# Performance work log

Measured on AMD Instinct MI355X. Metric: run time of the kernel, lower is better.

Reference implementation:

```python
import jax, jax.numpy as jnp
import numpy as np

N = 200000
B = 1024          # batch_size (number of graphs/segments)
D = 256           # in_channels
STEPS = 3         # processing_steps


def setup_inputs() -> dict:
    key = jax.random.key(0)
    ks = jax.random.split(key, 6)
    x = jax.random.normal(ks[0], (N, D), dtype=jnp.float32)
    bank_kg = jnp.zeros((1,), dtype=jnp.float32)  # unused by forward
    batch = jnp.sort(jax.random.randint(ks[1], (N,), 0, B, dtype=jnp.int32))
    q_star = jax.random.normal(ks[2], (B, 2 * D), dtype=jnp.float32)
    s = 1.0 / np.sqrt(D)  # PyTorch LSTM init scale
    W_ih = jax.random.uniform(ks[3], (4 * D, 2 * D), jnp.float32, -s, s)
    W_hh = jax.random.uniform(ks[4], (4 * D, D), jnp.float32, -s, s)
    b_ih = jnp.zeros((4 * D,), dtype=jnp.float32)
    b_hh = jnp.zeros((4 * D,), dtype=jnp.float32)
    return {"x": x, "bank_kg": bank_kg, "batch": batch, "q_star": q_star,
            "W_ih": W_ih, "W_hh": W_hh, "b_ih": b_ih, "b_hh": b_hh}


def _lstm_cell(inp, h, c, W_ih, W_hh, b_ih, b_hh):
    # PyTorch gate order: i, f, g, o
    gates = inp @ W_ih.T + b_ih + h @ W_hh.T + b_hh  # [B, 4D]
    i, f, g, o = jnp.split(gates, 4, axis=-1)
    i = jax.nn.sigmoid(i)
    f = jax.nn.sigmoid(f)
    g = jnp.tanh(g)
    o = jax.nn.sigmoid(o)
    c = f * c + i * g
    h = o * jnp.tanh(c)
    return h, c


def _segment_softmax(e, batch, num_segments):
    # numerically stable softmax over nodes grouped by segment id
    emax = jax.ops.segment_max(e, batch, num_segments=num_segments)
    emax = jnp.where(jnp.isfinite(emax), emax, 0.0)  # guard empty segments
    ee = jnp.exp(e - emax[batch])
    denom = jax.ops.segment_sum(ee, batch, num_segments=num_segments)
    return ee / (denom[batch] + 1e-16)


def reference(x, bank_kg, batch, q_star, W_ih, W_hh, b_ih, b_hh):
    del bank_kg  # unused in the original forward
    h = jnp.zeros((B, D), dtype=x.dtype)
    c = jnp.zeros((B, D), dtype=x.dtype)
    for _ in range(STEPS):
        h, c = _lstm_cell(q_star, h, c, W_ih, W_hh, b_ih, b_hh)
        q = h                                       # [B, D]
        e = jnp.sum(x * q[batch], axis=-1)          # [N] attention logits
        a = _segment_softmax(e, batch, B)           # [N]
        r = jax.ops.segment_sum(a[:, None] * x, batch, num_segments=B)  # [B, D]
        q_star = jnp.concatenate([q, r], axis=-1)   # [B, 2D]
    return q_star
```

## Files before the change

### kernel.cpp

```cpp
#include <hip/hip_runtime.h>
#include <hip/hip_bf16.h>
#include <cstdint>


#define NN     200000
#define BSEG   1024
#define DD     256
#define KA     768
#define FOURD  1024

using bf16x8 = __attribute__((ext_vector_type(8))) __bf16;
using f32x4  = __attribute__((ext_vector_type(4))) float;

__device__ __forceinline__ float bf2f(unsigned int u) {
  union { unsigned int i; float f; } v; v.i = (u & 0xffffu) << 16; return v.f;
}
__device__ __forceinline__ unsigned short f2bf(float f) {
  union { float f; unsigned int i; } v; v.f = f;
  unsigned int x = v.i;
  if ((x & 0x7fffffffu) > 0x7f800000u) return (unsigned short)((x >> 16) | 0x40);
  return (unsigned short)((x + 0x7fffu + ((x >> 16) & 1u)) >> 16);
}
__device__ __forceinline__ void split_bf(float f, unsigned short& hi, unsigned short& lo) {
  hi = f2bf(f);
  lo = f2bf(f - bf2f(hi));
}


__global__ void seg_bounds(const int* __restrict__ batch, int* __restrict__ segs) {
  int b = blockIdx.x * blockDim.x + threadIdx.x;
  if (b > BSEG) return;
  int lo = 0, hi = NN;
  while (lo < hi) { int mid = (lo + hi) >> 1; if (batch[mid] < b) lo = mid + 1; else hi = mid; }
  segs[b] = lo;
}

__global__ void prep_wcat(const float* __restrict__ Wih,
                          const float* __restrict__ Whh,
                          const float* __restrict__ bih,
                          const float* __restrict__ bhh,
                          unsigned short* __restrict__ Whi,
                          unsigned short* __restrict__ Wlo,
                          float* __restrict__ bias) {
  int idx = blockIdx.x * 256 + threadIdx.x;
  if (idx < FOURD * KA) {
    int j = idx / KA, k = idx - j * KA;
    float w = (k < 512) ? Wih[j * 512 + k] : Whh[j * 256 + (k - 512)];
    unsigned short hi, lo; split_bf(w, hi, lo);
    Whi[idx] = hi; Wlo[idx] = lo;
  }
  if (idx < FOURD) bias[idx] = bih[idx] + bhh[idx];
}

__global__ void prep_A(const float* __restrict__ qst,
                       unsigned short* __restrict__ Ahi,
                       unsigned short* __restrict__ Alo,
                       float* __restrict__ h, float* __restrict__ c) {
  int idx = blockIdx.x * 256 + threadIdx.x;
  if (idx >= BSEG * KA) return;
  int b = idx / KA, k = idx - b * KA;
  unsigned short hi = 0, lo = 0;
  if (k < 512) split_bf(qst[b * 512 + k], hi, lo);
  Ahi[idx] = hi; Alo[idx] = lo;
  if (k >= 512) { h[b * DD + (k - 512)] = 0.f; c[b * DD + (k - 512)] = 0.f; }
}

__global__ __launch_bounds__(256) void gemm_gates(const unsigned short* __restrict__ Ahi,
                                                  const unsigned short* __restrict__ Alo,
                                                  const unsigned short* __restrict__ Whi,
                                                  const unsigned short* __restrict__ Wlo,
                                                  float* __restrict__ gates) {
  int wave = (blockIdx.x << 2) | (threadIdx.x >> 6);
  int lane = threadIdx.x & 63;
  int m0 = (wave >> 6) << 4;
  int n0 = (wave & 63) << 4;
  int r16 = lane & 15, quad = lane >> 4;
  const unsigned short* ap  = Ahi + (size_t)(m0 + r16) * KA + quad * 8;
  const unsigned short* alp = Alo + (size_t)(m0 + r16) * KA + quad * 8;
  const unsigned short* bp  = Whi + (size_t)(n0 + r16) * KA + quad * 8;
  const unsigned short* blp = Wlo + (size_t)(n0 + r16) * KA + quad * 8;
  f32x4 acc = {0.f, 0.f, 0.f, 0.f};
  for (int k = 0; k < KA; k += 32) {
    bf16x8 a  = *(const bf16x8*)(ap + k);
    bf16x8 al = *(const bf16x8*)(alp + k);
    bf16x8 b  = *(const bf16x8*)(bp + k);
    bf16x8 bl = *(const bf16x8*)(blp + k);
    acc = __builtin_amdgcn_mfma_f32_16x16x32_bf16(a,  b,  acc, 0, 0, 0);
    acc = __builtin_amdgcn_mfma_f32_16x16x32_bf16(a,  bl, acc, 0, 0, 0);
    acc = __builtin_amdgcn_mfma_f32_16x16x32_bf16(al, b,  acc, 0, 0, 0);
  }
  #pragma unroll
  for (int r = 0; r < 4; ++r)
    gates[(size_t)(m0 + quad * 4 + r) * FOURD + n0 + r16] = acc[r];
}

__global__ __launch_bounds__(256) void lstm_pointwise(const float* __restrict__ gates,
                                                      const float* __restrict__ bias,
                                                      float* __restrict__ h,
                                                      float* __restrict__ c,
                                                      unsigned short* __restrict__ Ahi,
                                                      unsigned short* __restrict__ Alo,
                                                      float* __restrict__ qout) {
  int idx = blockIdx.x * 256 + threadIdx.x;
  int b = idx >> 8, d = idx & 255;
  const float* g = gates + (size_t)b * FOURD;
  float gi = g[d]       + bias[d];
  float gf = g[256 + d] + bias[256 + d];
  float gg = g[512 + d] + bias[512 + d];
  float go = g[768 + d] + bias[768 + d];
  float ig = 1.f / (1.f + expf(-gi));
  float fg = 1.f / (1.f + expf(-gf));
  float gt = tanhf(gg);
  float og = 1.f / (1.f + expf(-go));
  float cn = fg * c[idx] + ig * gt;
  float hn = og * tanhf(cn);
  c[idx] = cn; h[idx] = hn;
  unsigned short hi, lo; split_bf(hn, hi, lo);
  size_t ro = (size_t)b * KA;
  Ahi[ro + d] = hi;        Alo[ro + d] = lo;
  Ahi[ro + 512 + d] = hi;  Alo[ro + 512 + d] = lo;
  qout[(size_t)b * 512 + d] = hn;
}

__global__ __launch_bounds__(256) void attn_fused(const float* __restrict__ x,
                                                  const int* __restrict__ segs,
                                                  const float* __restrict__ h,
                                                  unsigned short* __restrict__ Ahi,
                                                  unsigned short* __restrict__ Alo,
                                                  float* __restrict__ qout) {
  int b = blockIdx.x;
  int t = threadIdx.x;
  int w = t >> 6, lane = t & 63;
  int s = segs[b], tend = segs[b + 1];

  float4 q = *(const float4*)(h + (size_t)b * DD + lane * 4);

  float m = -3.402823466e38f;
  float l = 0.f;
  float4 v = {0.f, 0.f, 0.f, 0.f};

  int i = s + w;
  float4 xv = {0.f, 0.f, 0.f, 0.f};
  if (i < tend) xv = *(const float4*)(x + (size_t)i * DD + lane * 4);
  for (; i < tend; i += 4) {
    float4 cur = xv;
    int nx = i + 4;
    if (nx < tend) xv = *(const float4*)(x + (size_t)nx * DD + lane * 4);
    float d = cur.x * q.x + cur.y * q.y + cur.z * q.z + cur.w * q.w;
    #pragma unroll
    for (int off = 32; off; off >>= 1) d += __shfl_xor(d, off);
    float mn = fmaxf(m, d);
    float alpha = __expf(m - mn);
    float wgt   = __expf(d - mn);
    l = l * alpha + wgt;
    v.x = v.x * alpha + wgt * cur.x;
    v.y = v.y * alpha + wgt * cur.y;
    v.z = v.z * alpha + wgt * cur.z;
    v.w = v.w * alpha + wgt * cur.w;
    m = mn;
  }

  __shared__ float sm[4], sl[4];
  __shared__ float sv[4][DD];
  if (lane == 0) { sm[w] = m; sl[w] = l; }
  *(float4*)(&sv[w][lane * 4]) = v;
  __syncthreads();

  float M = fmaxf(fmaxf(sm[0], sm[1]), fmaxf(sm[2], sm[3]));
  if (M < -1e37f) M = 0.f;
  float a0 = __expf(sm[0] - M), a1 = __expf(sm[1] - M);
  float a2 = __expf(sm[2] - M), a3 = __expf(sm[3] - M);
  float L = sl[0] * a0 + sl[1] * a1 + sl[2] * a2 + sl[3] * a3;
  float r = (sv[0][t] * a0 + sv[1][t] * a1 + sv[2][t] * a2 + sv[3][t] * a3)
            / (L + 1e-16f);

  unsigned short hi, lo; split_bf(r, hi, lo);
  size_t ro = (size_t)b * KA;
  Ahi[ro + DD + t] = hi;  Alo[ro + DD + t] = lo;
  qout[(size_t)b * 512 + DD + t] = r;
}

extern "C" void kernel_launch(void* const* d_in, const int* in_sizes, int n_in,
                              void* d_out, int out_size, void* d_ws, size_t ws_size,
                              hipStream_t stream) {
  const float* x    = (const float*)d_in[0];
  const int*   batc = (const int*)d_in[2];
  const float* qst  = (const float*)d_in[3];
  const float* Wih  = (const float*)d_in[4];
  const float* Whh  = (const float*)d_in[5];
  const float* bih  = (const float*)d_in[6];
  const float* bhh  = (const float*)d_in[7];
  float* out = (float*)d_out;

  char* ws = (char*)d_ws;
  size_t off = 0;
  auto alloc = [&](size_t bytes) -> void* {
    void* p = ws + off; off = (off + bytes + 255) & ~(size_t)255; return p;
  };
  int*            segs = (int*)alloc((size_t)(BSEG + 1) * 4);
  unsigned short* Whi  = (unsigned short*)alloc((size_t)FOURD * KA * 2);
  unsigned short* Wlo  = (unsigned short*)alloc((size_t)FOURD * KA * 2);
  unsigned short* Ahi  = (unsigned short*)alloc((size_t)BSEG * KA * 2);
  unsigned short* Alo  = (unsigned short*)alloc((size_t)BSEG * KA * 2);
  float*          gate = (float*)alloc((size_t)BSEG * FOURD * 4);
  float*          h    = (float*)alloc((size_t)BSEG * DD * 4);
  float*          c    = (float*)alloc((size_t)BSEG * DD * 4);
  float*          bias = (float*)alloc((size_t)FOURD * 4);

  seg_bounds<<<5, 256, 0, stream>>>(batc, segs);
  prep_wcat<<<(FOURD * KA + 255) / 256, 256, 0, stream>>>(Wih, Whh, bih, bhh, Whi, Wlo, bias);
  prep_A<<<(BSEG * KA + 255) / 256, 256, 0, stream>>>(qst, Ahi, Alo, h, c);

  for (int step = 0; step < 3; ++step) {
    gemm_gates<<<1024, 256, 0, stream>>>(Ahi, Alo, Whi, Wlo, gate);
    lstm_pointwise<<<BSEG * DD / 256, 256, 0, stream>>>(gate, bias, h, c, Ahi, Alo, out);
    attn_fused<<<BSEG, 256, 0, stream>>>(x, segs, h, Ahi, Alo, out);
  }
}
```

Before: 525.6 us.

## Fuse LSTM pointwise into attention, retile gates GEMM with LDS, merge prep kernels

Merges the three setup kernels into one launch. Retiles the gate GEMM so each block computes a 128x32 tile with the weight slice staged in XOR-swizzled shared memory and each wave doing a 2x2 grid of MFMA tiles, improving operand reuse. Folds the LSTM pointwise update into the attention kernel so h is passed through shared memory instead of a global buffer, removing one launch per step. The trade-off is fewer GEMM blocks (lower occupancy) and extra barriers in the GEMM loop.

Result: faster. 447.0 us (-14.9%).

```diff
diff --git a/kernel.cpp b/kernel.cpp
--- a/kernel.cpp
+++ b/kernel.cpp
@@ -26,43 +26,34 @@
   lo = f2bf(f - bf2f(hi));
 }
 
-
-__global__ void seg_bounds(const int* __restrict__ batch, int* __restrict__ segs) {
-  int b = blockIdx.x * blockDim.x + threadIdx.x;
-  if (b > BSEG) return;
-  int lo = 0, hi = NN;
-  while (lo < hi) { int mid = (lo + hi) >> 1; if (batch[mid] < b) lo = mid + 1; else hi = mid; }
-  segs[b] = lo;
-}
-
-__global__ void prep_wcat(const float* __restrict__ Wih,
-                          const float* __restrict__ Whh,
-                          const float* __restrict__ bih,
-                          const float* __restrict__ bhh,
-                          unsigned short* __restrict__ Whi,
-                          unsigned short* __restrict__ Wlo,
-                          float* __restrict__ bias) {
+__global__ void prep_all(const int* __restrict__ batch, int* __restrict__ segs,
+                         const float* __restrict__ Wih, const float* __restrict__ Whh,
+                         const float* __restrict__ bih, const float* __restrict__ bhh,
+                         unsigned short* __restrict__ Whi, unsigned short* __restrict__ Wlo,
+                         float* __restrict__ bias,
+                         const float* __restrict__ qst,
+                         unsigned short* __restrict__ Ahi, unsigned short* __restrict__ Alo,
+                         float* __restrict__ c) {
   int idx = blockIdx.x * 256 + threadIdx.x;
+  if (idx <= BSEG) {
+    int lo = 0, hi = NN;
+    while (lo < hi) { int mid = (lo + hi) >> 1; if (batch[mid] < idx) lo = mid + 1; else hi = mid; }
+    segs[idx] = lo;
+  }
+  if (idx < FOURD) bias[idx] = bih[idx] + bhh[idx];
   if (idx < FOURD * KA) {
     int j = idx / KA, k = idx - j * KA;
     float w = (k < 512) ? Wih[j * 512 + k] : Whh[j * 256 + (k - 512)];
     unsigned short hi, lo; split_bf(w, hi, lo);
     Whi[idx] = hi; Wlo[idx] = lo;
   }
-  if (idx < FOURD) bias[idx] = bih[idx] + bhh[idx];
-}
-
-__global__ void prep_A(const float* __restrict__ qst,
-                       unsigned short* __restrict__ Ahi,
-                       unsigned short* __restrict__ Alo,
-                       float* __restrict__ h, float* __restrict__ c) {
-  int idx = blockIdx.x * 256 + threadIdx.x;
-  if (idx >= BSEG * KA) return;
-  int b = idx / KA, k = idx - b * KA;
-  unsigned short hi = 0, lo = 0;
-  if (k < 512) split_bf(qst[b * 512 + k], hi, lo);
-  Ahi[idx] = hi; Alo[idx] = lo;
-  if (k >= 512) { h[b * DD + (k - 512)] = 0.f; c[b * DD + (k - 512)] = 0.f; }
+  if (idx < BSEG * KA) {
+    int b = idx / KA, k = idx - b * KA;
+    unsigned short hi = 0, lo = 0;
+    if (k < 512) split_bf(qst[b * 512 + k], hi, lo);
+    Ahi[idx] = hi; Alo[idx] = lo;
+  }
+  if (idx < BSEG * DD) c[idx] = 0.f;
 }
 
 __global__ __launch_bounds__(256) void gemm_gates(const unsigned short* __restrict__ Ahi,
@@ -70,70 +61,102 @@
                                                   const unsigned short* __restrict__ Whi,
                                                   const unsigned short* __restrict__ Wlo,
                                                   float* __restrict__ gates) {
-  int wave = (blockIdx.x << 2) | (threadIdx.x >> 6);
-  int lane = threadIdx.x & 63;
-  int m0 = (wave >> 6) << 4;
-  int n0 = (wave & 63) << 4;
+  int bx = blockIdx.x;
+  int m0 = (bx >> 5) << 7;
+  int n0 = (bx & 31) << 5;
+  int t = threadIdx.x, w = t >> 6, lane = t & 63;
   int r16 = lane & 15, quad = lane >> 4;
-  const unsigned short* ap  = Ahi + (size_t)(m0 + r16) * KA + quad * 8;
-  const unsigned short* alp = Alo + (size_t)(m0 + r16) * KA + quad * 8;
-  const unsigned short* bp  = Whi + (size_t)(n0 + r16) * KA + quad * 8;
-  const unsigned short* blp = Wlo + (size_t)(n0 + r16) * KA + quad * 8;
-  f32x4 acc = {0.f, 0.f, 0.f, 0.f};
-  for (int k = 0; k < KA; k += 32) {
-    bf16x8 a  = *(const bf16x8*)(ap + k);
-    bf16x8 al = *(const bf16x8*)(alp + k);
-    bf16x8 b  = *(const bf16x8*)(bp + k);
-    bf16x8 bl = *(const bf16x8*)(blp + k);
-    acc = __builtin_amdgcn_mfma_f32_16x16x32_bf16(a,  b,  acc, 0, 0, 0);
-    acc = __builtin_amdgcn_mfma_f32_16x16x32_bf16(a,  bl, acc, 0, 0, 0);
-    acc = __builtin_amdgcn_mfma_f32_16x16x32_bf16(al, b,  acc, 0, 0, 0);
+
+  __shared__ unsigned short sWhi[32 * 64];
+  __shared__ unsigned short sWlo[32 * 64];
+
+  f32x4 acc[2][2] = {};
+
+  const unsigned short* a0h = Ahi + (size_t)(m0 + 32 * w + r16) * KA + quad * 8;
+  const unsigned short* a0l = Alo + (size_t)(m0 + 32 * w + r16) * KA + quad * 8;
+
+  int srow = t >> 3;
+  int scb  = t & 7;
+  const unsigned short* gwh = Whi + (size_t)(n0 + srow) * KA + scb * 8;
+  const unsigned short* gwl = Wlo + (size_t)(n0 + srow) * KA + scb * 8;
+  int sdst = srow * 64 + ((scb ^ (srow & 7)) * 8);
+
+  for (int kc = 0; kc < KA; kc += 64) {
+    __syncthreads();
+    *(bf16x8*)&sWhi[sdst] = *(const bf16x8*)(gwh + kc);
+    *(bf16x8*)&sWlo[sdst] = *(const bf16x8*)(gwl + kc);
+    __syncthreads();
+    #pragma unroll
+    for (int ks = 0; ks < 2; ++ks) {
+      bf16x8 bh[2], bl[2];
+      #pragma unroll
+      for (int ni = 0; ni < 2; ++ni) {
+        int wr = 16 * ni + r16;
+        int off = wr * 64 + (((ks * 4 + quad) ^ (wr & 7)) * 8);
+        bh[ni] = *(const bf16x8*)&sWhi[off];
+        bl[ni] = *(const bf16x8*)&sWlo[off];
+      }
+      #pragma unroll
+      for (int ms = 0; ms < 2; ++ms) {
+        bf16x8 a  = *(const bf16x8*)(a0h + (size_t)ms * 16 * KA + kc + ks * 32);
+        bf16x8 al = *(const bf16x8*)(a0l + (size_t)ms * 16 * KA + kc + ks * 32);
+        #pragma unroll
+        for (int ni = 0; ni < 2; ++ni) {
+          acc[ms][ni] = __builtin_amdgcn_mfma_f32_16x16x32_bf16(a,  bh[ni], acc[ms][ni], 0, 0, 0);
+          acc[ms][ni] = __builtin_amdgcn_mfma_f32_16x16x32_bf16(a,  bl[ni], acc[ms][ni], 0, 0, 0);
+          acc[ms][ni] = __builtin_amdgcn_mfma_f32_16x16x32_bf16(al, bh[ni], acc[ms][ni], 0, 0, 0);
+        }
+      }
+    }
   }
   #pragma unroll
-  for (int r = 0; r < 4; ++r)
-    gates[(size_t)(m0 + quad * 4 + r) * FOURD + n0 + r16] = acc[r];
-}
-
-__global__ __launch_bounds__(256) void lstm_pointwise(const float* __restrict__ gates,
-                                                      const float* __restrict__ bias,
-                                                      float* __restrict__ h,
-                                                      float* __restrict__ c,
-                                                      unsigned short* __restrict__ Ahi,
-                                                      unsigned short* __restrict__ Alo,
-                                                      float* __restrict__ qout) {
-  int idx = blockIdx.x * 256 + threadIdx.x;
-  int b = idx >> 8, d = idx & 255;
+  for (int ms = 0; ms < 2; ++ms)
+    #pragma unroll
+    for (int ni = 0; ni < 2; ++ni)
+      #pragma unroll
+      for (int r = 0; r < 4; ++r)
+        gates[(size_t)(m0 + 32 * w + 16 * ms + quad * 4 + r) * FOURD
+              + n0 + 16 * ni + r16] = acc[ms][ni][r];
+}
+
+__global__ __launch_bounds__(256) void attn_fused(const float* __restrict__ x,
+                                                  const int* __restrict__ segs,
+                                                  const float* __restrict__ gates,
+                                                  const float* __restrict__ bias,
+                                                  float* __restrict__ c,
+                                                  unsigned short* __restrict__ Ahi,
+                                                  unsigned short* __restrict__ Alo,
+                                                  float* __restrict__ qout) {
+  int b = blockIdx.x, t = threadIdx.x;
+  int w = t >> 6, lane = t & 63;
+
   const float* g = gates + (size_t)b * FOURD;
-  float gi = g[d]       + bias[d];
-  float gf = g[256 + d] + bias[256 + d];
-  float gg = g[512 + d] + bias[512 + d];
-  float go = g[768 + d] + bias[768 + d];
+  float gi = g[t]       + bias[t];
+  float gf = g[256 + t] + bias[256 + t];
+  float gg = g[512 + t] + bias[512 + t];
+  float go = g[768 + t] + bias[768 + t];
   float ig = 1.f / (1.f + expf(-gi));
   float fg = 1.f / (1.f + expf(-gf));
   float gt = tanhf(gg);
   float og = 1.f / (1.f + expf(-go));
-  float cn = fg * c[idx] + ig * gt;
+  int cidx = b * DD + t;
+  float cn = fg * c[cidx] + ig * gt;
+  c[cidx] = cn;
   float hn = og * tanhf(cn);
-  c[idx] = cn; h[idx] = hn;
-  unsigned short hi, lo; split_bf(hn, hi, lo);
-  size_t ro = (size_t)b * KA;
-  Ahi[ro + d] = hi;        Alo[ro + d] = lo;
-  Ahi[ro + 512 + d] = hi;  Alo[ro + 512 + d] = lo;
-  qout[(size_t)b * 512 + d] = hn;
-}
-
-__global__ __launch_bounds__(256) void attn_fused(const float* __restrict__ x,
-                                                  const int* __restrict__ segs,
-                                                  const float* __restrict__ h,
-                                                  unsigned short* __restrict__ Ahi,
-                                                  unsigned short* __restrict__ Alo,
-                                                  float* __restrict__ qout) {
-  int b = blockIdx.x;
-  int t = threadIdx.x;
-  int w = t >> 6, lane = t & 63;
+
+  __shared__ __align__(16) float sh[DD];
+  sh[t] = hn;
+  {
+    unsigned short hi, lo; split_bf(hn, hi, lo);
+    size_t ro = (size_t)b * KA;
+    Ahi[ro + t] = hi;        Alo[ro + t] = lo;
+    Ahi[ro + 512 + t] = hi;  Alo[ro + 512 + t] = lo;
+    qout[(size_t)b * 512 + t] = hn;
+  }
+  __syncthreads();
+
   int s = segs[b], tend = segs[b + 1];
-
-  float4 q = *(const float4*)(h + (size_t)b * DD + lane * 4);
+  float4 q = *(const float4*)(sh + lane * 4);
 
   float m = -3.402823466e38f;
   float l = 0.f;
@@ -161,7 +184,7 @@
   }
 
   __shared__ float sm[4], sl[4];
-  __shared__ float sv[4][DD];
+  __shared__ __align__(16) float sv[4][DD];
   if (lane == 0) { sm[w] = m; sl[w] = l; }
   *(float4*)(&sv[w][lane * 4]) = v;
   __syncthreads();
@@ -203,17 +226,14 @@
   unsigned short* Ahi  = (unsigned short*)alloc((size_t)BSEG * KA * 2);
   unsigned short* Alo  = (unsigned short*)alloc((size_t)BSEG * KA * 2);
   float*          gate = (float*)alloc((size_t)BSEG * FOURD * 4);
-  float*          h    = (float*)alloc((size_t)BSEG * DD * 4);
   float*          c    = (float*)alloc((size_t)BSEG * DD * 4);
   float*          bias = (float*)alloc((size_t)FOURD * 4);
 
-  seg_bounds<<<5, 256, 0, stream>>>(batc, segs);
-  prep_wcat<<<(FOURD * KA + 255) / 256, 256, 0, stream>>>(Wih, Whh, bih, bhh, Whi, Wlo, bias);
-  prep_A<<<(BSEG * KA + 255) / 256, 256, 0, stream>>>(qst, Ahi, Alo, h, c);
+  prep_all<<<(FOURD * KA + 255) / 256, 256, 0, stream>>>(
+      batc, segs, Wih, Whh, bih, bhh, Whi, Wlo, bias, qst, Ahi, Alo, c);
 
   for (int step = 0; step < 3; ++step) {
-    gemm_gates<<<1024, 256, 0, stream>>>(Ahi, Alo, Whi, Wlo, gate);
-    lstm_pointwise<<<BSEG * DD / 256, 256, 0, stream>>>(gate, bias, h, c, Ahi, Alo, out);
-    attn_fused<<<BSEG, 256, 0, stream>>>(x, segs, h, Ahi, Alo, out);
-  }
-}
+    gemm_gates<<<256, 256, 0, stream>>>(Ahi, Alo, Whi, Wlo, gate);
+    attn_fused<<<BSEG, 256, 0, stream>>>(x, segs, gate, bias, c, Ahi, Alo, out);
+  }
+}
```
